# Kernel tuning notes

Measured on AMD Instinct MI355X. Metric: run time of the kernel, lower is better.

The kernel has to match this reference:

```python
import jax, jax.numpy as jnp
import numpy as np

N_NODES = 50000
N_EDGES = 800000
IN_CH = 128
HID = 128
OUT_CH = 6
N_GRAPHS = 64


def setup_inputs() -> dict:
    key = jax.random.key(0)
    ks = jax.random.split(key, 12)
    x = jax.random.normal(ks[0], (N_NODES, IN_CH), dtype=jnp.float32)
    edge_index = jax.random.randint(ks[1], (2, N_EDGES), 0, N_NODES, dtype=jnp.int64)
    batch = jnp.sort(jax.random.randint(ks[2], (N_NODES,), 0, N_GRAPHS, dtype=jnp.int64))
    def glorot(k, fan_in, fan_out):
        lim = float(np.sqrt(6.0 / (fan_in + fan_out)))
        return jax.random.uniform(k, (fan_in, fan_out), dtype=jnp.float32, minval=-lim, maxval=lim)
    W0 = glorot(ks[3], IN_CH, HID); b0 = jnp.zeros((HID,), jnp.float32)
    W1 = glorot(ks[4], HID, HID);   b1 = jnp.zeros((HID,), jnp.float32)
    W2 = glorot(ks[5], HID, HID);   b2 = jnp.zeros((HID,), jnp.float32)
    Wl = glorot(ks[6], HID, OUT_CH); bl = jnp.zeros((OUT_CH,), jnp.float32)
    return {"x": x, "edge_index": edge_index, "batch": batch,
            "W0": W0, "b0": b0, "W1": W1, "b1": b1, "W2": W2, "b2": b2,
            "Wl": Wl, "bl": bl}


def _gcn_conv(x, src, dst, norm_src_dst, norm_self, W, b):
    # PyG GCNConv: h = x @ W; out[i] = sum_{j->i} n_j n_i h[j] + n_i^2 h[i] + b
    h = x @ W                                   # [N, out]
    msg = h[src] * norm_src_dst[:, None]        # [E, out] gather + scale
    agg = jax.ops.segment_sum(msg, dst, num_segments=N_NODES)
    agg = agg + h * norm_self[:, None]          # self-loop contribution
    return agg + b


def reference(x, edge_index, batch, W0, b0, W1, b1, W2, b2, Wl, bl):
    src, dst = edge_index[0], edge_index[1]
    # symmetric normalization with self-loops (edge weight 1)
    deg = jax.ops.segment_sum(jnp.ones((N_EDGES,), x.dtype), dst, num_segments=N_NODES) + 1.0
    dinv = jax.lax.rsqrt(deg)                   # deg >= 1 so safe
    norm_sd = dinv[src] * dinv[dst]             # per-edge norm
    norm_self = dinv * dinv                     # per-node self-loop norm

    h = jnp.tanh(_gcn_conv(x, src, dst, norm_sd, norm_self, W0, b0))
    h = jnp.tanh(_gcn_conv(h, src, dst, norm_sd, norm_self, W1, b1))
    h = jnp.tanh(_gcn_conv(h, src, dst, norm_sd, norm_self, W2, b2))

    h = jnp.tanh(h @ Wl + bl)                   # per-node linear + act

    # global mean pool per graph
    sums = jax.ops.segment_sum(h, batch, num_segments=N_GRAPHS)
    counts = jax.ops.segment_sum(jnp.ones((N_NODES,), h.dtype), batch, num_segments=N_GRAPHS)
    return sums / jnp.maximum(counts, 1.0)[:, None]
```

## Files before the change

### kernel.cpp

```cpp
#include <hip/hip_runtime.h>
#include <hip/hip_fp16.h>

#define NN 50000
#define EE 800000
#define CH 128
#define NGR 64
#define NB 196

__global__ __launch_bounds__(256) void count_deg(const int* __restrict__ dst,
                                                 int* __restrict__ counts) {
  int e = blockIdx.x * 256 + threadIdx.x;
  if (e < EE) atomicAdd(&counts[dst[e]], 1);
}

__global__ __launch_bounds__(256) void scan_block_sums(const int* __restrict__ counts,
                                                       int* __restrict__ blockSums) {
  __shared__ int red[256];
  int t = threadIdx.x;
  int i = blockIdx.x * 256 + t;
  red[t] = (i < NN) ? counts[i] : 0;
  __syncthreads();
  for (int off = 128; off > 0; off >>= 1) {
    if (t < off) red[t] += red[t + off];
    __syncthreads();
  }
  if (t == 0) blockSums[blockIdx.x] = red[0];
}

__global__ __launch_bounds__(256) void scan_final(const int* __restrict__ counts,
                                                  const int* __restrict__ blockSums,
                                                  int* __restrict__ rowptr,
                                                  int* __restrict__ fillptr,
                                                  float* __restrict__ dinv) {
  __shared__ int tmp[256];
  __shared__ int sOffs[256];
  int t = threadIdx.x;
  int bs = (t < NB) ? blockSums[t] : 0;
  sOffs[t] = bs;
  __syncthreads();
  for (int off = 1; off < 256; off <<= 1) {
    int add = (t >= off) ? sOffs[t - off] : 0;
    __syncthreads();
    sOffs[t] += add;
    __syncthreads();
  }
  int myBlockOff = sOffs[blockIdx.x] - blockSums[blockIdx.x];

  int i = blockIdx.x * 256 + t;
  int v = (i < NN) ? counts[i] : 0;
  tmp[t] = v;
  __syncthreads();
  for (int off = 1; off < 256; off <<= 1) {
    int add = (t >= off) ? tmp[t - off] : 0;
    __syncthreads();
    tmp[t] += add;
    __syncthreads();
  }
  if (i < NN) {
    int ex = myBlockOff + tmp[t] - v;
    rowptr[i] = ex;
    fillptr[i] = ex;
    dinv[i] = rsqrtf((float)v + 1.0f);
  }
  if (i == 0) rowptr[NN] = EE;
}

__global__ __launch_bounds__(256) void fill_csr(const int* __restrict__ src,
                                                const int* __restrict__ dst,
                                                const float* __restrict__ dinv,
                                                int* __restrict__ fillptr,
                                                int2* __restrict__ edges) {
  int e = blockIdx.x * 256 + threadIdx.x;
  if (e >= EE) return;
  int s = src[e], d = dst[e];
  int slot = atomicAdd(&fillptr[d], 1);
  edges[slot] = make_int2(s, __float_as_int(dinv[s] * dinv[d]));
}

__global__ __launch_bounds__(256) void gemm128(const float* __restrict__ X,
                                               const float* __restrict__ W,
                                               __half* __restrict__ H16) {
  __shared__ float sW[64 * 128];
  __shared__ float sX[64 * 64];
  float4* sW4 = (float4*)sW;
  float4* sX4 = (float4*)sX;
  const float4* X4 = (const float4*)X;
  const float4* W4 = (const float4*)W;
  int t = threadIdx.x;
  int row0 = blockIdx.x * 64;
  int lane = t & 31;
  int rowg = t >> 5;

  float acc[8][4];
  #pragma unroll
  for (int r = 0; r < 8; ++r)
    #pragma unroll
    for (int c = 0; c < 4; ++c) acc[r][c] = 0.f;

  for (int kt = 0; kt < 2; ++kt) {
    __syncthreads();
    #pragma unroll
    for (int i = 0; i < 8; ++i) {
      int idx = t + 256 * i;
      sW4[idx] = W4[kt * 2048 + idx];
    }
    #pragma unroll
    for (int i = 0; i < 4; ++i) {
      int idx = t + 256 * i;
      int row = row0 + (idx >> 4);
      int c4 = idx & 15;
      float4 v = make_float4(0.f, 0.f, 0.f, 0.f);
      if (row < NN) v = X4[(size_t)row * 32 + kt * 16 + c4];
      sX4[idx] = v;
    }
    __syncthreads();
    #pragma unroll
    for (int k4 = 0; k4 < 16; ++k4) {
      float4 xv[8];
      #pragma unroll
      for (int r = 0; r < 8; ++r)
        xv[r] = sX4[(rowg * 8 + r) * 16 + k4];
      #pragma unroll
      for (int kk = 0; kk < 4; ++kk) {
        float4 wv = sW4[(k4 * 4 + kk) * 32 + lane];
        #pragma unroll
        for (int r = 0; r < 8; ++r) {
          float xs = (kk == 0) ? xv[r].x : (kk == 1) ? xv[r].y : (kk == 2) ? xv[r].z : xv[r].w;
          acc[r][0] += xs * wv.x;
          acc[r][1] += xs * wv.y;
          acc[r][2] += xs * wv.z;
          acc[r][3] += xs * wv.w;
        }
      }
    }
  }

  #pragma unroll
  for (int r = 0; r < 8; ++r) {
    int row = row0 + rowg * 8 + r;
    if (row < NN) {
      __half2 p0 = __floats2half2_rn(acc[r][0], acc[r][1]);
      __half2 p1 = __floats2half2_rn(acc[r][2], acc[r][3]);
      uint2 u = make_uint2(*(unsigned*)&p0, *(unsigned*)&p1);
      ((uint2*)H16)[(size_t)row * 32 + lane] = u;
    }
  }
}

__global__ __launch_bounds__(256) void gcn_agg(const __half* __restrict__ H16,
                                               const int* __restrict__ rowptr,
                                               const int2* __restrict__ edges,
                                               const float* __restrict__ dinv,
                                               const float* __restrict__ bias,
                                               float* __restrict__ out) {
  int nid = blockIdx.x * 4 + (threadIdx.x >> 6);
  if (nid >= NN) return;
  int lane = threadIdx.x & 63;
  const __half2* Hh = (const __half2*)H16;
  float di = dinv[nid];
  float sw = di * di;
  float2 self = __half22float2(Hh[(size_t)nid * 64 + lane]);
  float ax = self.x * sw, ay = self.y * sw;

  int e0 = rowptr[nid], e1 = rowptr[nid + 1];
  for (int c = e0; c < e1; c += 64) {
    int2 rec = (c + lane < e1) ? edges[c + lane] : make_int2(0, 0);
    int cnt = e1 - c; if (cnt > 64) cnt = 64;
    int cend = (cnt + 15) & ~15;
    for (int u = 0; u < cend; u += 16) {
      __half2 v[16];
      float wg[16];
      #pragma unroll
      for (int q = 0; q < 16; ++q) {
        int s  = __builtin_amdgcn_readlane(rec.x, u + q);
        wg[q]  = __int_as_float(__builtin_amdgcn_readlane(rec.y, u + q));
        v[q]   = Hh[(size_t)s * 64 + lane];
      }
      #pragma unroll
      for (int q = 0; q < 16; ++q) {
        float2 f = __half22float2(v[q]);
        ax += f.x * wg[q];
        ay += f.y * wg[q];
      }
    }
  }

  float2 b = ((const float2*)bias)[lane];
  float2 r;
  r.x = tanhf(ax + b.x);
  r.y = tanhf(ay + b.y);
  ((float2*)out)[(size_t)nid * 64 + lane] = r;
}

__global__ __launch_bounds__(256) void linpool(const float* __restrict__ H,
                                               const float* __restrict__ Wl,
                                               const float* __restrict__ bl,
                                               const int* __restrict__ batch,
                                               float* __restrict__ gsum,
                                               int* __restrict__ gcnt) {
  __shared__ float sW[128 * 6];
  __shared__ float sSum[NGR * 6];
  __shared__ int sCnt[NGR];
  int t = threadIdx.x;
  for (int i = t; i < 768; i += 256) sW[i] = Wl[i];
  for (int i = t; i < NGR * 6; i += 256) sSum[i] = 0.f;
  if (t < NGR) sCnt[t] = 0;
  __syncthreads();

  int gid = blockIdx.x * 256 + t;
  int node = gid >> 2;
  int seg = gid & 3;
  float a0 = 0, a1 = 0, a2 = 0, a3 = 0, a4 = 0, a5 = 0;
  if (node < NN) {
    const float4* H4 = (const float4*)(H + (size_t)node * 128 + seg * 32);
    #pragma unroll
    for (int q = 0; q < 8; ++q) {
      float4 hv = H4[q];
      float hvv[4] = {hv.x, hv.y, hv.z, hv.w};
      int kbase = seg * 32 + q * 4;
      #pragma unroll
      for (int kk = 0; kk < 4; ++kk) {
        float hx = hvv[kk];
        const float* wr = &sW[(kbase + kk) * 6];
        a0 += hx * wr[0]; a1 += hx * wr[1]; a2 += hx * wr[2];
        a3 += hx * wr[3]; a4 += hx * wr[4]; a5 += hx * wr[5];
      }
    }
  }
  a0 += __shfl_xor(a0, 1); a0 += __shfl_xor(a0, 2);
  a1 += __shfl_xor(a1, 1); a1 += __shfl_xor(a1, 2);
  a2 += __shfl_xor(a2, 1); a2 += __shfl_xor(a2, 2);
  a3 += __shfl_xor(a3, 1); a3 += __shfl_xor(a3, 2);
  a4 += __shfl_xor(a4, 1); a4 += __shfl_xor(a4, 2);
  a5 += __shfl_xor(a5, 1); a5 += __shfl_xor(a5, 2);
  if (node < NN && seg == 0) {
    int g = batch[node];
    atomicAdd(&sSum[g * 6 + 0], tanhf(a0 + bl[0]));
    atomicAdd(&sSum[g * 6 + 1], tanhf(a1 + bl[1]));
    atomicAdd(&sSum[g * 6 + 2], tanhf(a2 + bl[2]));
    atomicAdd(&sSum[g * 6 + 3], tanhf(a3 + bl[3]));
    atomicAdd(&sSum[g * 6 + 4], tanhf(a4 + bl[4]));
    atomicAdd(&sSum[g * 6 + 5], tanhf(a5 + bl[5]));
    atomicAdd(&sCnt[g], 1);
  }
  __syncthreads();
  for (int i = t; i < NGR * 6; i += 256) {
    int g = i / 6;
    if (sCnt[g] > 0) atomicAdd(&gsum[i], sSum[i]);
  }
  if (t < NGR && sCnt[t] > 0) atomicAdd(&gcnt[t], sCnt[t]);
}

__global__ void finalize(const float* __restrict__ gsum, const int* __restrict__ gcnt,
                         float* __restrict__ out) {
  int i = threadIdx.x;
  if (i < NGR * 6) {
    int g = i / 6;
    float c = (float)max(gcnt[g], 1);
    out[i] = gsum[i] / c;
  }
}

extern "C" void kernel_launch(void* const* d_in, const int* in_sizes, int n_in,
                              void* d_out, int out_size, void* d_ws, size_t ws_size,
                              hipStream_t stream) {
  const float* x  = (const float*)d_in[0];
  const int*   ei = (const int*)d_in[1];
  const int*   batch = (const int*)d_in[2];
  const float* W0 = (const float*)d_in[3];
  const float* b0 = (const float*)d_in[4];
  const float* W1 = (const float*)d_in[5];
  const float* b1 = (const float*)d_in[6];
  const float* W2 = (const float*)d_in[7];
  const float* b2 = (const float*)d_in[8];
  const float* Wl = (const float*)d_in[9];
  const float* bl = (const float*)d_in[10];
  float* out = (float*)d_out;

  const int* src = ei;
  const int* dst = ei + EE;

  char* w = (char*)d_ws;
  auto alloc = [&](size_t bytes) {
    void* p = (void*)w;
    w += (bytes + 255) & ~(size_t)255;
    return p;
  };
  float*  bufA   = (float*)alloc((size_t)NN * CH * 4);
  float*  bufB   = (float*)alloc((size_t)NN * CH * 4);
  __half* h16    = (__half*)alloc((size_t)NN * CH * 2);
  int*    counts = (int*)alloc((size_t)NN * 4);
  int*    rowptr = (int*)alloc((size_t)(NN + 1) * 4);
  int*    fillptr= (int*)alloc((size_t)NN * 4);
  float*  dinv   = (float*)alloc((size_t)NN * 4);
  int2*   edges  = (int2*)alloc((size_t)EE * 8);
  int*    blockSums = (int*)alloc(256 * 4);
  float*  gsum   = (float*)alloc((NGR * 6 + NGR) * 4);
  int*    gcnt   = (int*)(gsum + NGR * 6);

  hipMemsetAsync(counts, 0, (size_t)NN * 4, stream);
  hipMemsetAsync(gsum, 0, (NGR * 6 + NGR) * 4, stream);

  count_deg<<<(EE + 255) / 256, 256, 0, stream>>>(dst, counts);
  scan_block_sums<<<NB, 256, 0, stream>>>(counts, blockSums);
  scan_final<<<NB, 256, 0, stream>>>(counts, blockSums, rowptr, fillptr, dinv);
  fill_csr<<<(EE + 255) / 256, 256, 0, stream>>>(src, dst, dinv, fillptr, edges);

  const int gemmGrid = (NN + 63) / 64;
  const int aggGrid  = (NN + 3) / 4;

  gemm128<<<gemmGrid, 256, 0, stream>>>(x, W0, h16);
  gcn_agg<<<aggGrid, 256, 0, stream>>>(h16, rowptr, edges, dinv, b0, bufA);
  gemm128<<<gemmGrid, 256, 0, stream>>>(bufA, W1, h16);
  gcn_agg<<<aggGrid, 256, 0, stream>>>(h16, rowptr, edges, dinv, b1, bufB);
  gemm128<<<gemmGrid, 256, 0, stream>>>(bufB, W2, h16);
  gcn_agg<<<aggGrid, 256, 0, stream>>>(h16, rowptr, edges, dinv, b2, bufA);

  linpool<<<(NN * 4 + 255) / 256, 256, 0, stream>>>(bufA, Wl, bl, batch, gsum, gcnt);
  finalize<<<1, NGR * 6, 0, stream>>>(gsum, gcnt, out);
}
```

Baseline: 367.4 us.

## Replace FP32 SIMT GEMM with fp16 MFMA using prepacked weight fragments

Replaces the shared-memory FP32 FMA GEMM with a matrix-core kernel using mfma_f32_16x16x32_f16. Each wave loads its 16 input rows straight from global memory and converts them to fp16. A new pre-pass packs all three weight matrices into per-lane fp16 fragments, so the GEMM reads B operands directly without LDS staging. This cuts GEMM compute time but lowers input and weight precision to fp16, and the output stores become scattered 2-byte writes.

```diff
diff --git a/kernel.cpp b/kernel.cpp
--- a/kernel.cpp
+++ b/kernel.cpp
@@ -6,6 +6,9 @@
 #define CH 128
 #define NGR 64
 #define NB 196
+
+typedef _Float16 half8 __attribute__((ext_vector_type(8)));
+typedef float floatx4 __attribute__((ext_vector_type(4)));
 
 __global__ __launch_bounds__(256) void count_deg(const int* __restrict__ dst,
                                                  int* __restrict__ counts) {
@@ -77,72 +80,70 @@
   edges[slot] = make_int2(s, __float_as_int(dinv[s] * dinv[d]));
 }
 
-__global__ __launch_bounds__(256) void gemm128(const float* __restrict__ X,
-                                               const float* __restrict__ W,
-                                               __half* __restrict__ H16) {
-  __shared__ float sW[64 * 128];
-  __shared__ float sX[64 * 64];
-  float4* sW4 = (float4*)sW;
-  float4* sX4 = (float4*)sX;
-  const float4* X4 = (const float4*)X;
-  const float4* W4 = (const float4*)W;
+__global__ __launch_bounds__(256) void w2frag(const float* __restrict__ W0,
+                                              const float* __restrict__ W1,
+                                              const float* __restrict__ W2,
+                                              half8* __restrict__ Wfrag) {
+  int slot = blockIdx.x * 256 + threadIdx.x;
+  if (slot >= 3 * 2048) return;
+  const float* W = (slot < 2048) ? W0 : (slot < 4096) ? W1 : W2;
+  int s = slot & 2047;
+  int lane = s & 63;
+  int fb = s >> 6;
+  int ks = fb >> 3, ct = fb & 7;
+  int kg = lane >> 4;
+  int col = ct * 16 + (lane & 15);
+  int kbase = ks * 32 + kg * 8;
+  half8 h;
+  #pragma unroll
+  for (int j = 0; j < 8; ++j) h[j] = (_Float16)W[(kbase + j) * CH + col];
+  Wfrag[slot] = h;
+}
+
+__global__ __launch_bounds__(256) void gemm_mfma(const float* __restrict__ X,
+                                                 const half8* __restrict__ Wfrag,
+                                                 __half* __restrict__ H16) {
   int t = threadIdx.x;
-  int row0 = blockIdx.x * 64;
-  int lane = t & 31;
-  int rowg = t >> 5;
-
-  float acc[8][4];
-  #pragma unroll
-  for (int r = 0; r < 8; ++r)
+  int wave = t >> 6, lane = t & 63;
+  int r0 = blockIdx.x * 64 + wave * 16;
+  int row = r0 + (lane & 15);
+  int kg = lane >> 4;
+  bool valid = row < NN;
+  const float4* Xr = (const float4*)(X + (size_t)row * CH);
+
+  half8 a[4];
+  #pragma unroll
+  for (int ks = 0; ks < 4; ++ks) {
+    float4 f0 = make_float4(0.f, 0.f, 0.f, 0.f), f1 = f0;
+    if (valid) { f0 = Xr[ks * 8 + kg * 2]; f1 = Xr[ks * 8 + kg * 2 + 1]; }
+    half8 h;
+    h[0] = (_Float16)f0.x; h[1] = (_Float16)f0.y; h[2] = (_Float16)f0.z; h[3] = (_Float16)f0.w;
+    h[4] = (_Float16)f1.x; h[5] = (_Float16)f1.y; h[6] = (_Float16)f1.z; h[7] = (_Float16)f1.w;
+    a[ks] = h;
+  }
+
+  floatx4 acc[8];
+  #pragma unroll
+  for (int ct = 0; ct < 8; ++ct) acc[ct] = (floatx4){0.f, 0.f, 0.f, 0.f};
+
+  #pragma unroll
+  for (int ct = 0; ct < 8; ++ct) {
     #pragma unroll
-    for (int c = 0; c < 4; ++c) acc[r][c] = 0.f;
-
-  for (int kt = 0; kt < 2; ++kt) {
-    __syncthreads();
+    for (int ks = 0; ks < 4; ++ks) {
+      half8 b = Wfrag[(ks * 8 + ct) * 64 + lane];
+      acc[ct] = __builtin_amdgcn_mfma_f32_16x16x32_f16(a[ks], b, acc[ct], 0, 0, 0);
+    }
+  }
+
+  int orow = r0 + (lane >> 4) * 4;
+  int ocol = lane & 15;
+  #pragma unroll
+  for (int ct = 0; ct < 8; ++ct) {
     #pragma unroll
-    for (int i = 0; i < 8; ++i) {
-      int idx = t + 256 * i;
-      sW4[idx] = W4[kt * 2048 + idx];
-    }
-    #pragma unroll
-    for (int i = 0; i < 4; ++i) {
-      int idx = t + 256 * i;
-      int row = row0 + (idx >> 4);
-      int c4 = idx & 15;
-      float4 v = make_float4(0.f, 0.f, 0.f, 0.f);
-      if (row < NN) v = X4[(size_t)row * 32 + kt * 16 + c4];
-      sX4[idx] = v;
-    }
-    __syncthreads();
-    #pragma unroll
-    for (int k4 = 0; k4 < 16; ++k4) {
-      float4 xv[8];
-      #pragma unroll
-      for (int r = 0; r < 8; ++r)
-        xv[r] = sX4[(rowg * 8 + r) * 16 + k4];
-      #pragma unroll
-      for (int kk = 0; kk < 4; ++kk) {
-        float4 wv = sW4[(k4 * 4 + kk) * 32 + lane];
-        #pragma unroll
-        for (int r = 0; r < 8; ++r) {
-          float xs = (kk == 0) ? xv[r].x : (kk == 1) ? xv[r].y : (kk == 2) ? xv[r].z : xv[r].w;
-          acc[r][0] += xs * wv.x;
-          acc[r][1] += xs * wv.y;
-          acc[r][2] += xs * wv.z;
-          acc[r][3] += xs * wv.w;
-        }
-      }
-    }
-  }
-
-  #pragma unroll
-  for (int r = 0; r < 8; ++r) {
-    int row = row0 + rowg * 8 + r;
-    if (row < NN) {
-      __half2 p0 = __floats2half2_rn(acc[r][0], acc[r][1]);
-      __half2 p1 = __floats2half2_rn(acc[r][2], acc[r][3]);
-      uint2 u = make_uint2(*(unsigned*)&p0, *(unsigned*)&p1);
-      ((uint2*)H16)[(size_t)row * 32 + lane] = u;
+    for (int r = 0; r < 4; ++r) {
+      int rr = orow + r;
+      if (rr < NN)
+        H16[(size_t)rr * CH + ct * 16 + ocol] = __float2half(acc[ct][r]);
     }
   }
 }
@@ -289,6 +290,7 @@
   float*  bufA   = (float*)alloc((size_t)NN * CH * 4);
   float*  bufB   = (float*)alloc((size_t)NN * CH * 4);
   __half* h16    = (__half*)alloc((size_t)NN * CH * 2);
+  half8*  wfrag  = (half8*)alloc((size_t)3 * 2048 * 16);
   int*    counts = (int*)alloc((size_t)NN * 4);
   int*    rowptr = (int*)alloc((size_t)(NN + 1) * 4);
   int*    fillptr= (int*)alloc((size_t)NN * 4);
@@ -305,15 +307,16 @@
   scan_block_sums<<<NB, 256, 0, stream>>>(counts, blockSums);
   scan_final<<<NB, 256, 0, stream>>>(counts, blockSums, rowptr, fillptr, dinv);
   fill_csr<<<(EE + 255) / 256, 256, 0, stream>>>(src, dst, dinv, fillptr, edges);
+  w2frag<<<24, 256, 0, stream>>>(W0, W1, W2, wfrag);
 
   const int gemmGrid = (NN + 63) / 64;
   const int aggGrid  = (NN + 3) / 4;
 
-  gemm128<<<gemmGrid, 256, 0, stream>>>(x, W0, h16);
+  gemm_mfma<<<gemmGrid, 256, 0, stream>>>(x, wfrag, h16);
   gcn_agg<<<aggGrid, 256, 0, stream>>>(h16, rowptr, edges, dinv, b0, bufA);
-  gemm128<<<gemmGrid, 256, 0, stream>>>(bufA, W1, h16);
+  gemm_mfma<<<gemmGrid, 256, 0, stream>>>(bufA, wfrag + 2048, h16);
   gcn_agg<<<aggGrid, 256, 0, stream>>>(h16, rowptr, edges, dinv, b1, bufB);
-  gemm128<<<gemmGrid, 256, 0, stream>>>(bufB, W2, h16);
+  gemm_mfma<<<gemmGrid, 256, 0, stream>>>(bufB, wfrag + 4096, h16);
   gcn_agg<<<aggGrid, 256, 0, stream>>>(h16, rowptr, edges, dinv, b2, bufA);
 
   linpool<<<(NN * 4 + 255) / 256, 256, 0, stream>>>(bufA, Wl, bl, batch, gsum, gcnt);
```

Measured after the change: 318.4 us. 1.15x faster.
